# Performance work log

Hardware: AMD Instinct MI355X
Metric: run time of the kernel (lower is better)

Reference implementation:

```python
import jax, jax.numpy as jnp
import numpy as np
from jax import lax

DWT_SCALE = 0.5
IDWT_SCALE = 1.0
PAD = 2  # (kernel_size-1)//2 for k=5


def haar_dwt(x, s):
    """x: [B,C,H,W] -> (ll, lh, hl, hh) each [B,C,H/2,W/2]. 2x2 Haar, scale s."""
    a = x[..., 0::2, 0::2]
    b = x[..., 0::2, 1::2]
    c = x[..., 1::2, 0::2]
    d = x[..., 1::2, 1::2]
    ll = s * (a + b + c + d)
    lh = s * (a + b - c - d)
    hl = s * (a - b + c - d)
    hh = s * (a - b - c + d)
    return ll, lh, hl, hh


def haar_idwt(ll, lh, hl, hh, s):
    """Inverse of haar_dwt when s_dwt * s_idwt_total = 0.5. Returns [B,C,2H,2W]."""
    a = s * (ll + lh + hl + hh)
    b = s * (ll + lh - hl - hh)
    c = s * (ll - lh + hl - hh)
    d = s * (ll - lh - hl + hh)
    B, C, H2, W2 = ll.shape
    top = jnp.stack([a, b], axis=-1).reshape(B, C, H2, 2 * W2)  # even rows
    bot = jnp.stack([c, d], axis=-1).reshape(B, C, H2, 2 * W2)  # odd rows
    return jnp.stack([top, bot], axis=-2).reshape(B, C, 2 * H2, 2 * W2)


def conv2d(x, w, pad):
    return lax.conv_general_dilated(
        x, w, window_strides=(1, 1), padding=[(pad, pad), (pad, pad)],
        dimension_numbers=("NCHW", "OIHW", "NCHW"))


def setup_inputs() -> dict:
    key = jax.random.key(0)
    kx, k0, k1, k2, kb = jax.random.split(key, 5)
    C, K = 64, 5
    x = jax.random.normal(kx, (8, C, 256, 256), dtype=jnp.float32)
    # kaiming_uniform-ish small init to keep 3-level recursion numerically tame
    scale = 0.02
    w0 = jax.random.normal(k0, (4 * C, 4 * C, K, K), dtype=jnp.float32) * scale
    w1 = jax.random.normal(k1, (4 * C, 4 * C, K, K), dtype=jnp.float32) * scale
    w2 = jax.random.normal(k2, (4 * C, 4 * C, K, K), dtype=jnp.float32) * scale
    bias = jax.random.normal(kb, (C,), dtype=jnp.float32) * 0.01
    return {"x": x, "w0": w0, "w1": w1, "w2": w2, "bias": bias}


def reference(x, w0, w1, w2, bias):
    weights = [w0, w1, w2]
    idwt_s = DWT_SCALE * IDWT_SCALE  # perfect reconstruction pair
    curr = x
    ll_levels, high_levels = [], []
    for w in weights:
        ll, lh, hl, hh = haar_dwt(curr, DWT_SCALE)
        curr = ll  # pre-conv LL feeds the next level
        B, C, H2, W2 = ll.shape
        stacked = jnp.stack([ll, lh, hl, hh], axis=2).reshape(B, 4 * C, H2, W2)
        y = conv2d(stacked, w, PAD)  # [B, 4*Co, H2, W2]
        y = y.reshape(B, -1, 4, H2, W2)
        ll_levels.append(y[:, :, 0])
        high_levels.append(y[:, :, 1:])
    next_ll = jnp.zeros_like(ll_levels[-1])
    for ll_t, h_t in zip(reversed(ll_levels), reversed(high_levels)):
        ll = ll_t + next_ll
        next_ll = haar_idwt(ll, h_t[:, :, 0], h_t[:, :, 1], h_t[:, :, 2], idwt_s)
    return next_ll + bias.reshape(1, -1, 1, 1)
```

## Files before the change

### kernel.cpp

```cpp
#include <hip/hip_runtime.h>


typedef unsigned short u16;
typedef __attribute__((ext_vector_type(8))) __bf16 bf16x8;
typedef __attribute__((ext_vector_type(4))) float f32x4;

__device__ __forceinline__ u16 f2bf(float f) {
  union { float f; unsigned u; } v; v.f = f;
  unsigned r = v.u + 0x7fffu + ((v.u >> 16) & 1u);
  return (u16)(r >> 16);
}
__device__ __forceinline__ float bf2f(u16 u) {
  union { unsigned u; float f; } v; v.u = ((unsigned)u) << 16;
  return v.f;
}

typedef const unsigned int __attribute__((address_space(1)))* gas1_t;
typedef unsigned int __attribute__((address_space(3)))* gas3_t;
__device__ __forceinline__ void gload16(const void* g, void* l) {
  __builtin_amdgcn_global_load_lds((gas1_t)g, (gas3_t)l, 16, 0, 0);
}

__global__ void k_wtrans(const float* __restrict__ w, u16* __restrict__ wb) {
  int co = blockIdx.x;
  int ci = threadIdx.x;
  const float* src = w + ((long)co * 256 + ci) * 25;
  float v[25];
#pragma unroll
  for (int tp = 0; tp < 25; ++tp) v[tp] = src[tp];
#pragma unroll
  for (int tp = 0; tp < 25; ++tp)
    wb[((long)tp * 256 + co) * 256 + ci] = f2bf(v[tp]);
}

__global__ void k_border(u16* __restrict__ st, int B_, int H2, int W2) {
  int PW = W2 + 4;
  int npix = 4 * PW + 4 * H2;
  int gid = blockIdx.x * blockDim.x + threadIdx.x;
  int pid = gid >> 6, lane = gid & 63;
  if (pid >= B_ * npix) return;
  int b = pid / npix, p = pid % npix;
  int row, col;
  if (p < 2 * PW) { row = p / PW; col = p % PW; }
  else if (p < 4 * PW) { int q = p - 2 * PW; row = H2 + 2 + q / PW; col = q % PW; }
  else { int q = p - 4 * PW; row = 2 + (q >> 2); int c4 = q & 3; col = (c4 < 2) ? c4 : W2 + c4; }
  long base = (((long)b * (H2 + 4) + row) * PW + col) * 256 + lane * 4;
  *(ushort4*)(st + base) = make_ushort4(0, 0, 0, 0);
}

__global__ void k_dwt(const float* __restrict__ in, u16* __restrict__ st,
                      float* __restrict__ ll, int B_, int H2, int W2) {
  int idx = blockIdx.x * blockDim.x + threadIdx.x;
  int W2h = W2 >> 1;
  int total = B_ * 64 * H2 * W2h;
  if (idx >= total) return;
  int w2h = idx % W2h; int t2 = idx / W2h;
  int h2 = t2 % H2; t2 /= H2;
  int c = t2 % 64; int b = t2 / 64;
  int w2 = w2h * 2;
  const float* r0 = in + (((long)(b * 64 + c) * (2 * H2) + 2 * h2) * (2 * W2)) + 2 * w2;
  const float* r1 = r0 + 2 * W2;
  float4 tp = *(const float4*)r0;
  float4 bt = *(const float4*)r1;
  float ll0 = 0.5f * (tp.x + tp.y + bt.x + bt.y);
  float lh0 = 0.5f * (tp.x + tp.y - bt.x - bt.y);
  float hl0 = 0.5f * (tp.x - tp.y + bt.x - bt.y);
  float hh0 = 0.5f * (tp.x - tp.y - bt.x + bt.y);
  float ll1 = 0.5f * (tp.z + tp.w + bt.z + bt.w);
  float lh1 = 0.5f * (tp.z + tp.w - bt.z - bt.w);
  float hl1 = 0.5f * (tp.z - tp.w + bt.z - bt.w);
  float hh1 = 0.5f * (tp.z - tp.w - bt.z + bt.w);
  long sbase = (((long)b * (H2 + 4) + (h2 + 2)) * (W2 + 4) + (w2 + 2)) * 256 + 4 * c;
  *(ushort4*)(st + sbase)       = make_ushort4(f2bf(ll0), f2bf(lh0), f2bf(hl0), f2bf(hh0));
  *(ushort4*)(st + sbase + 256) = make_ushort4(f2bf(ll1), f2bf(lh1), f2bf(hl1), f2bf(hh1));
  long lbase = (((long)(b * 64 + c) * H2) + h2) * W2 + w2;
  *(float2*)(ll + lbase) = make_float2(ll0, ll1);
}

__global__ __launch_bounds__(512, 1) void k_conv8(
    const u16* __restrict__ st, const u16* __restrict__ wt, u16* __restrict__ y,
    int H2, int W2) {
  __shared__ __align__(16) char smem[131072];
  const int t = threadIdx.x;
  const int lane = t & 63;
  const int wv = t >> 6;
  const int wm = wv >> 2, wn = wv & 3;
  const int nwg = gridDim.x;
  const int bid = blockIdx.x;
  const int lb = (bid & 7) * (nwg >> 3) + (bid >> 3);
  const int m0 = lb * 256;
  const int PW = W2 + 4;

  const int trow = t >> 3;
  const int srcci = ((t & 7) ^ (trow & 7)) * 8;
  const char* baseA[4];
#pragma unroll
  for (int u = 0; u < 4; ++u) {
    int m = m0 + u * 64 + trow;
    int w = m % W2; int q = m / W2;
    int hh = q % H2; int b = q / H2;
    long sp = ((long)(b * (H2 + 4) + hh + 2) * PW + (w + 2));
    baseA[u] = (const char*)(st + sp * 256 + srcci);
  }
  const char* baseB0 = (const char*)(wt + trow * 256 + srcci);

  f32x4 acc[8][4];
#pragma unroll
  for (int i = 0; i < 8; ++i)
#pragma unroll
    for (int j = 0; j < 4; ++j) acc[i][j] = f32x4{0.f, 0.f, 0.f, 0.f};

  const int kq = (lane >> 4) * 16;
  const int sw = (lane & 7) << 4;
  const int kx0 = (kq) ^ sw;
  const int kx1 = (64 + kq) ^ sw;
  const int aBase = (wm * 128 + (lane & 15)) * 128;
  const int bBase = 32768 + (wn * 64 + (lane & 15)) * 128;

  auto stageA = [&](int kt, char* dst, int up) {
    int tap = kt >> 2, cic = kt & 3;
    int dy = tap / 5 - 2, dx = tap % 5 - 2;
    long off = ((long)(dy * PW + dx) * 256 + cic * 64) * 2;
#pragma unroll
    for (int u = up * 2; u < up * 2 + 2; ++u)
      gload16(baseA[u] + off, dst + u * 8192 + wv * 1024);
  };
  auto stageB = [&](int kt, char* dst, int up) {
    int tap = kt >> 2, cic = kt & 3;
    long off = ((long)tap * 65536 + cic * 64) * 2;
#pragma unroll
    for (int u = up * 2; u < up * 2 + 2; ++u)
      gload16(baseB0 + u * 32768 + off, dst + 32768 + u * 8192 + wv * 1024);
  };

#define QMFMA(mh, nh)                                                              \
  _Pragma("unroll") for (int i = 0; i < 4; ++i)                                    \
  _Pragma("unroll") for (int jj = 0; jj < 2; ++jj)                                 \
  _Pragma("unroll") for (int ks = 0; ks < 2; ++ks)                                 \
    acc[(mh)*4 + i][(nh)*2 + jj] = __builtin_amdgcn_mfma_f32_16x16x32_bf16(        \
        af[mh][i][ks], bfr[jj][ks], acc[(mh)*4 + i][(nh)*2 + jj], 0, 0, 0);

  stageA(0, smem, 0); stageA(0, smem, 1);
  stageB(0, smem, 0); stageB(0, smem, 1);
  stageA(1, smem + 65536, 0); stageA(1, smem + 65536, 1);
  asm volatile("s_waitcnt vmcnt(4)" ::: "memory");
  __builtin_amdgcn_s_barrier();

  for (int kt = 0; kt < 100; ++kt) {
    char* bufp = smem + (kt & 1) * 65536;
    char* altp = smem + ((kt & 1) ^ 1) * 65536;
    bf16x8 af[2][4][2], bfr[2][2];
#pragma unroll
    for (int i = 0; i < 4; ++i) {
      af[0][i][0] = *(const bf16x8*)(bufp + aBase + i * 2048 + kx0);
      af[0][i][1] = *(const bf16x8*)(bufp + aBase + i * 2048 + kx1);
    }
#pragma unroll
    for (int jj = 0; jj < 2; ++jj) {
      bfr[jj][0] = *(const bf16x8*)(bufp + bBase + jj * 2048 + kx0);
      bfr[jj][1] = *(const bf16x8*)(bufp + bBase + jj * 2048 + kx1);
    }
    if (kt + 1 < 100) stageB(kt + 1, altp, 0);
    __builtin_amdgcn_s_barrier();
    asm volatile("s_waitcnt lgkmcnt(0)" ::: "memory");
    __builtin_amdgcn_sched_barrier(0);
    __builtin_amdgcn_s_setprio(1);
    QMFMA(0, 0)
    __builtin_amdgcn_s_setprio(0);
    __builtin_amdgcn_s_barrier();
#pragma unroll
    for (int i = 0; i < 4; ++i) {
      af[1][i][0] = *(const bf16x8*)(bufp + aBase + (4 + i) * 2048 + kx0);
      af[1][i][1] = *(const bf16x8*)(bufp + aBase + (4 + i) * 2048 + kx1);
    }
    if (kt + 1 < 100) stageB(kt + 1, altp, 1);
    __builtin_amdgcn_s_barrier();
    asm volatile("s_waitcnt lgkmcnt(0)" ::: "memory");
    __builtin_amdgcn_sched_barrier(0);
    __builtin_amdgcn_s_setprio(1);
    QMFMA(1, 0)
    __builtin_amdgcn_s_setprio(0);
    __builtin_amdgcn_s_barrier();
#pragma unroll
    for (int jj = 0; jj < 2; ++jj) {
      bfr[jj][0] = *(const bf16x8*)(bufp + bBase + (2 + jj) * 2048 + kx0);
      bfr[jj][1] = *(const bf16x8*)(bufp + bBase + (2 + jj) * 2048 + kx1);
    }
    if (kt + 2 < 100) stageA(kt + 2, bufp, 0);
    __builtin_amdgcn_s_barrier();
    asm volatile("s_waitcnt lgkmcnt(0)" ::: "memory");
    __builtin_amdgcn_sched_barrier(0);
    __builtin_amdgcn_s_setprio(1);
    QMFMA(0, 1)
    __builtin_amdgcn_s_setprio(0);
    __builtin_amdgcn_s_barrier();
    if (kt + 2 < 100) stageA(kt + 2, bufp, 1);
    __builtin_amdgcn_s_barrier();
    __builtin_amdgcn_s_setprio(1);
    QMFMA(1, 1)
    __builtin_amdgcn_s_setprio(0);
    if (kt < 98) { asm volatile("s_waitcnt vmcnt(4)" ::: "memory"); }
    else if (kt == 98) { asm volatile("s_waitcnt vmcnt(0)" ::: "memory"); }
    __builtin_amdgcn_s_barrier();
  }
#undef QMFMA

#pragma unroll
  for (int i = 0; i < 8; ++i) {
    int mloc = m0 + wm * 128 + i * 16 + (lane >> 4) * 4;
#pragma unroll
    for (int j = 0; j < 4; ++j) {
      int nloc = wn * 64 + j * 16 + (lane & 15);
#pragma unroll
      for (int r = 0; r < 4; ++r)
        y[(long)(mloc + r) * 256 + nloc] = f2bf(acc[i][j][r]);
    }
  }
}

__global__ __launch_bounds__(512, 1) void k_conv_p(
    const u16* __restrict__ st, const u16* __restrict__ wt, u16* __restrict__ y,
    int H2, int W2) {
  __shared__ __align__(16) char smem[147456];
  const int t = threadIdx.x;
  const int lane = t & 63;
  const int wv = t >> 6;
  const int wm = wv >> 2;
  const int wn = wv & 3;
  const int nwg = gridDim.x;
  const int bid = blockIdx.x;
  const int lb = (bid & 7) * (nwg >> 3) + (bid >> 3);
  const int m0 = lb * 128;
  const int PW = W2 + 4;

  const int trow = t >> 3;
  const int srcci = ((t & 7) ^ (trow & 7)) * 8;
  const char* baseA[2];
  const char* baseB[4];
#pragma unroll
  for (int h = 0; h < 2; ++h) {
    int m = m0 + h * 64 + trow;
    int w = m % W2; int q = m / W2;
    int hh = q % H2; int b = q / H2;
    long sp = ((long)(b * (H2 + 4) + hh + 2) * PW + (w + 2));
    baseA[h] = (const char*)(st + sp * 256 + srcci);
  }
#pragma unroll
  for (int u = 0; u < 4; ++u) {
    int n = u * 64 + trow;
    baseB[u] = (const char*)(wt + (long)n * 256 + srcci);
  }

  f32x4 acc[4][4];
#pragma unroll
  for (int i = 0; i < 4; ++i)
#pragma unroll
    for (int j = 0; j < 4; ++j) acc[i][j] = f32x4{0.f, 0.f, 0.f, 0.f};

  const int kq = (lane >> 4) * 16;
  int aoff[2][4], boff[2][4];
#pragma unroll
  for (int ks = 0; ks < 2; ++ks)
#pragma unroll
    for (int i = 0; i < 4; ++i) {
      int ra = wm * 64 + i * 16 + (lane & 15);
      int kb = ks * 64 + kq;
      aoff[ks][i] = ra * 128 + (kb ^ ((ra & 7) << 4));
      int rb = wn * 64 + i * 16 + (lane & 15);
      boff[ks][i] = 16384 + rb * 128 + (kb ^ ((rb & 7) << 4));
    }

  auto stage_a = [&](int kt) {
    int tap = kt >> 2, cic = kt & 3;
    int dy = tap / 5 - 2, dx = tap % 5 - 2;
    long offA = ((long)(dy * PW + dx) * 256 + cic * 64) * 2;
    long offB = ((long)tap * 65536 + cic * 64) * 2;
    char* lb2 = smem + (kt % 3) * 49152 + wv * 1024;
    gload16(baseA[0] + offA, lb2);
    gload16(baseA[1] + offA, lb2 + 8192);
    gload16(baseB[0] + offB, lb2 + 16384);
  };
  auto stage_b = [&](int kt) {
    int tap = kt >> 2, cic = kt & 3;
    long offB = ((long)tap * 65536 + cic * 64) * 2;
    char* lb2 = smem + (kt % 3) * 49152 + wv * 1024;
    gload16(baseB[1] + offB, lb2 + 24576);
    gload16(baseB[2] + offB, lb2 + 32768);
    gload16(baseB[3] + offB, lb2 + 40960);
  };

  stage_a(0); stage_b(0);
  stage_a(1); stage_b(1);
  asm volatile("s_waitcnt vmcnt(6)" ::: "memory");
  __builtin_amdgcn_s_barrier();

  for (int kt = 0; kt < 100; ++kt) {
    const char* la = smem + (kt % 3) * 49152;
    const bool st2 = (kt + 2) < 100;
    bf16x8 af[4], bfr[4];
#pragma unroll
    for (int i = 0; i < 4; ++i) af[i] = *(const bf16x8*)(la + aoff[0][i]);
#pragma unroll
    for (int j = 0; j < 4; ++j) bfr[j] = *(const bf16x8*)(la + boff[0][j]);
    if (st2) stage_a(kt + 2);
    __builtin_amdgcn_s_barrier();
    asm volatile("s_waitcnt lgkmcnt(0)" ::: "memory");
    __builtin_amdgcn_sched_barrier(0);
    __builtin_amdgcn_s_setprio(1);
#pragma unroll
    for (int i = 0; i < 4; ++i)
#pragma unroll
      for (int j = 0; j < 4; ++j)
        acc[i][j] = __builtin_amdgcn_mfma_f32_16x16x32_bf16(af[i], bfr[j], acc[i][j], 0, 0, 0);
    __builtin_amdgcn_s_setprio(0);
    __builtin_amdgcn_s_barrier();
#pragma unroll
    for (int i = 0; i < 4; ++i) af[i] = *(const bf16x8*)(la + aoff[1][i]);
#pragma unroll
    for (int j = 0; j < 4; ++j) bfr[j] = *(const bf16x8*)(la + boff[1][j]);
    if (st2) stage_b(kt + 2);
    __builtin_amdgcn_s_barrier();
    asm volatile("s_waitcnt lgkmcnt(0)" ::: "memory");
    __builtin_amdgcn_sched_barrier(0);
    __builtin_amdgcn_s_setprio(1);
#pragma unroll
    for (int i = 0; i < 4; ++i)
#pragma unroll
      for (int j = 0; j < 4; ++j)
        acc[i][j] = __builtin_amdgcn_mfma_f32_16x16x32_bf16(af[i], bfr[j], acc[i][j], 0, 0, 0);
    __builtin_amdgcn_s_setprio(0);
    if (st2) {
      asm volatile("s_waitcnt vmcnt(6)" ::: "memory");
    } else if (kt + 1 < 100) {
      asm volatile("s_waitcnt vmcnt(0)" ::: "memory");
    }
    __builtin_amdgcn_s_barrier();
  }

#pragma unroll
  for (int i = 0; i < 4; ++i) {
    int mloc = m0 + wm * 64 + i * 16 + (lane >> 4) * 4;
#pragma unroll
    for (int j = 0; j < 4; ++j) {
      int nloc = wn * 64 + j * 16 + (lane & 15);
#pragma unroll
      for (int r = 0; r < 4; ++r)
        y[(long)(mloc + r) * 256 + nloc] = f2bf(acc[i][j][r]);
    }
  }
}

__global__ __launch_bounds__(256) void k_conv(
    const u16* __restrict__ st, const u16* __restrict__ wt, u16* __restrict__ y,
    int H2, int W2) {
  __shared__ __align__(16) char smem[32768];
  const int t = threadIdx.x;
  const int lane = t & 63;
  const int wv = t >> 6;
  const int wm = wv >> 1, wn = wv & 1;
  const int m0 = blockIdx.x * 128;
  const int n0 = blockIdx.y * 128;
  const int PW = W2 + 4;
  const int lsub = lane & 7;
  const int lrow8 = lane >> 3;
  const int srcci = (lsub ^ lrow8) * 8;

  const char* baseA[4];
  const char* baseB[4];
#pragma unroll
  for (int l = 0; l < 4; ++l) {
    int ml = (wv * 4 + l) * 8 + lrow8;
    int m = m0 + ml;
    int w = m % W2;
    int q = m / W2;
    int h = q % H2;
    int b = q / H2;
    long sp = ((long)(b * (H2 + 4) + h + 2) * PW + (w + 2));
    baseA[l] = (const char*)(st + sp * 256 + srcci);
    int nl = n0 + (wv * 4 + l) * 8 + lrow8;
    baseB[l] = (const char*)(wt + (long)nl * 256 + srcci);
  }

  f32x4 acc[4][4];
#pragma unroll
  for (int i = 0; i < 4; ++i)
#pragma unroll
    for (int j = 0; j < 4; ++j) acc[i][j] = f32x4{0.f, 0.f, 0.f, 0.f};

  const int arow = wm * 64 + (lane & 15);
  const int brow = wn * 64 + (lane & 15);
  const int kq = (lane >> 4) * 16;
  int aoff[2][4], boff[2][4];
#pragma unroll
  for (int ks = 0; ks < 2; ++ks)
#pragma unroll
    for (int i = 0; i < 4; ++i) {
      int ra = arow + i * 16;
      int kb = ks * 64 + kq;
      aoff[ks][i] = ra * 128 + (kb ^ ((ra & 7) << 4));
      int rb = brow + i * 16;
      boff[ks][i] = 16384 + rb * 128 + (kb ^ ((rb & 7) << 4));
    }

  for (int kk = 0; kk < 100; ++kk) {
    const int tap = kk >> 2, cic = kk & 3;
    const int dy = tap / 5 - 2, dx = tap % 5 - 2;
    const int offA = ((dy * PW + dx) * 256 + cic * 64) * 2;
    const int offB = (tap * 65536 + cic * 64) * 2;
#pragma unroll
    for (int l = 0; l < 4; ++l) {
      gload16(baseA[l] + offA, smem + (wv * 4 + l) * 1024);
      gload16(baseB[l] + offB, smem + 16384 + (wv * 4 + l) * 1024);
    }
    __syncthreads();
#pragma unroll
    for (int ks = 0; ks < 2; ++ks) {
      bf16x8 af[4], bfr[4];
#pragma unroll
      for (int i = 0; i < 4; ++i) af[i] = *(const bf16x8*)(smem + aoff[ks][i]);
#pragma unroll
      for (int j = 0; j < 4; ++j) bfr[j] = *(const bf16x8*)(smem + boff[ks][j]);
#pragma unroll
      for (int i = 0; i < 4; ++i)
#pragma unroll
        for (int j = 0; j < 4; ++j)
          acc[i][j] = __builtin_amdgcn_mfma_f32_16x16x32_bf16(af[i], bfr[j], acc[i][j], 0, 0, 0);
    }
    __syncthreads();
  }

  const long ybase = (long)m0 * 256 + n0;
#pragma unroll
  for (int i = 0; i < 4; ++i) {
    int mloc = wm * 64 + i * 16 + (lane >> 4) * 4;
#pragma unroll
    for (int j = 0; j < 4; ++j) {
      int nloc = wn * 64 + j * 16 + (lane & 15);
#pragma unroll
      for (int r = 0; r < 4; ++r)
        y[ybase + (long)(mloc + r) * 256 + nloc] = f2bf(acc[i][j][r]);
    }
  }
}

__global__ void k_idwt(const u16* __restrict__ y, const float* __restrict__ nll,
                       float* __restrict__ out, const float* __restrict__ bias,
                       int B_, int H2, int W2) {
  int idx = blockIdx.x * blockDim.x + threadIdx.x;
  int W2h = W2 >> 1;
  int total = B_ * 64 * H2 * W2h;
  if (idx >= total) return;
  int w2h = idx % W2h; int t2 = idx / W2h;
  int h2 = t2 % H2; t2 /= H2;
  int c = t2 % 64; int b = t2 / 64;
  int w2 = w2h * 2;
  long ybase = (((long)b * H2 + h2) * W2 + w2) * 256 + 4 * c;
  ushort4 q0 = *(const ushort4*)(y + ybase);
  ushort4 q1 = *(const ushort4*)(y + ybase + 256);
  float llv0 = bf2f(q0.x), lh0 = bf2f(q0.y), hl0 = bf2f(q0.z), hh0 = bf2f(q0.w);
  float llv1 = bf2f(q1.x), lh1 = bf2f(q1.y), hl1 = bf2f(q1.z), hh1 = bf2f(q1.w);
  if (nll) {
    float2 nv = *(const float2*)(nll + (((long)(b * 64 + c) * H2 + h2) * W2 + w2));
    llv0 += nv.x; llv1 += nv.y;
  }
  float bv = bias ? bias[c] : 0.f;
  float a0 = 0.5f * (llv0 + lh0 + hl0 + hh0) + bv;
  float b0 = 0.5f * (llv0 + lh0 - hl0 - hh0) + bv;
  float c0 = 0.5f * (llv0 - lh0 + hl0 - hh0) + bv;
  float d0 = 0.5f * (llv0 - lh0 - hl0 + hh0) + bv;
  float a1 = 0.5f * (llv1 + lh1 + hl1 + hh1) + bv;
  float b1 = 0.5f * (llv1 + lh1 - hl1 - hh1) + bv;
  float c1 = 0.5f * (llv1 - lh1 + hl1 - hh1) + bv;
  float d1 = 0.5f * (llv1 - lh1 - hl1 + hh1) + bv;
  long obase = (((long)(b * 64 + c) * (2 * H2) + 2 * h2) * (2 * W2)) + 2 * w2;
  *(float4*)(out + obase)          = make_float4(a0, b0, a1, b1);
  *(float4*)(out + obase + 2 * W2) = make_float4(c0, d0, c1, d1);
}

constexpr size_t WBF_SZ1 = 25ull * 256 * 256 * 2;
constexpr size_t OFF_WBF = 0;
constexpr size_t OFF_S0  = 3 * WBF_SZ1;
constexpr size_t S0_SZ   = 8ull * 132 * 132 * 256 * 2;
constexpr size_t REL_S1 = 0;
constexpr size_t S1_SZ  = 8ull * 68 * 68 * 256 * 2;
constexpr size_t REL_L1 = REL_S1 + S1_SZ;
constexpr size_t L1_SZ  = 8ull * 64 * 64 * 64 * 4;
constexpr size_t REL_S2 = REL_L1 + L1_SZ;
constexpr size_t S2_SZ  = 8ull * 36 * 36 * 256 * 2;
constexpr size_t REL_Y1 = REL_S2 + S2_SZ;
constexpr size_t Y1_SZ  = 8ull * 64 * 64 * 256 * 2;
constexpr size_t REL_Y2 = REL_Y1 + Y1_SZ;
constexpr size_t Y2_SZ  = 8ull * 32 * 32 * 256 * 2;
constexpr size_t REL_N2 = REL_Y2 + Y2_SZ;
constexpr size_t N2_SZ  = 8ull * 64 * 64 * 64 * 4;
constexpr size_t REL_L2 = REL_N2 + N2_SZ;
constexpr size_t OFF_L0 = OFF_S0 + S0_SZ;
constexpr size_t L0_SZ  = 8ull * 64 * 128 * 128 * 4;
constexpr size_t OFF_Y0 = OFF_L0 + L0_SZ;
constexpr size_t Y0_SZ  = 8ull * 128 * 128 * 256 * 2;

extern "C" void kernel_launch(void* const* d_in, const int* in_sizes, int n_in,
                              void* d_out, int out_size, void* d_ws, size_t ws_size,
                              hipStream_t stream) {
  const float* x    = (const float*)d_in[0];
  const float* w0   = (const float*)d_in[1];
  const float* w1   = (const float*)d_in[2];
  const float* w2   = (const float*)d_in[3];
  const float* bias = (const float*)d_in[4];
  float* out = (float*)d_out;
  char* ws = (char*)d_ws;

  u16* wbf0 = (u16*)(ws + OFF_WBF);
  u16* wbf1 = (u16*)(ws + OFF_WBF + WBF_SZ1);
  u16* wbf2 = (u16*)(ws + OFF_WBF + 2 * WBF_SZ1);
  u16* s0 = (u16*)(ws + OFF_S0);
  u16* s1 = (u16*)(ws + OFF_S0 + REL_S1);
  float* l1 = (float*)(ws + OFF_S0 + REL_L1);
  u16* s2 = (u16*)(ws + OFF_S0 + REL_S2);
  u16* y1 = (u16*)(ws + OFF_S0 + REL_Y1);
  u16* y2 = (u16*)(ws + OFF_S0 + REL_Y2);
  float* n2 = (float*)(ws + OFF_S0 + REL_N2);
  float* l2 = (float*)(ws + OFF_S0 + REL_L2);
  float* l0 = (float*)(ws + OFF_L0);
  float* n1 = (float*)(ws + OFF_L0);
  u16* y0 = (u16*)(ws + OFF_Y0);

  k_wtrans<<<256, 256, 0, stream>>>(w0, wbf0);
  k_wtrans<<<256, 256, 0, stream>>>(w1, wbf1);
  k_wtrans<<<256, 256, 0, stream>>>(w2, wbf2);

  k_border<<<2080, 256, 0, stream>>>(s0, 8, 128, 128);
  k_dwt<<<16384, 256, 0, stream>>>(x, s0, l0, 8, 128, 128);
  k_conv8<<<512, 512, 0, stream>>>(s0, wbf0, y0, 128, 128);

  k_border<<<1056, 256, 0, stream>>>(s1, 8, 64, 64);
  k_border<<<544, 256, 0, stream>>>(s2, 8, 32, 32);

  k_dwt<<<4096, 256, 0, stream>>>(l0, s1, l1, 8, 64, 64);
  k_conv_p<<<256, 512, 0, stream>>>(s1, wbf1, y1, 64, 64);

  k_dwt<<<1024, 256, 0, stream>>>(l1, s2, l2, 8, 32, 32);
  k_conv<<<dim3(64, 2), 256, 0, stream>>>(s2, wbf2, y2, 32, 32);

  k_idwt<<<1024, 256, 0, stream>>>(y2, nullptr, n2, nullptr, 8, 32, 32);
  k_idwt<<<4096, 256, 0, stream>>>(y1, n2, n1, nullptr, 8, 64, 64);
  k_idwt<<<16384, 256, 0, stream>>>(y0, n1, out, bias, 8, 128, 128);
}
```

Baseline: 741.6 us.

## Prefetch next k-tile fragments into registers and reorder MFMA quadrants to cut barriers

Restructures the conv GEMM main loop. LDS fragments for the next k-tile are loaded at the end of the current tile, and the quadrant order is changed so A and B fragments are reused across adjacent MFMA groups. Some barriers and full lgkmcnt waits are removed or relaxed, and per-iteration tap/div math becomes incremental offset updates. The last two iterations are peeled to drop the bounds checks. This costs more live registers and adds risk around the LDS reuse ordering.

```diff
diff --git a/kernel.cpp b/kernel.cpp
--- a/kernel.cpp
+++ b/kernel.cpp
@@ -112,98 +112,112 @@
 
   const int kq = (lane >> 4) * 16;
   const int sw = (lane & 7) << 4;
-  const int kx0 = (kq) ^ sw;
+  const int kx0 = kq ^ sw;
   const int kx1 = (64 + kq) ^ sw;
   const int aBase = (wm * 128 + (lane & 15)) * 128;
   const int bBase = 32768 + (wn * 64 + (lane & 15)) * 128;
 
-  auto stageA = [&](int kt, char* dst, int up) {
-    int tap = kt >> 2, cic = kt & 3;
-    int dy = tap / 5 - 2, dx = tap % 5 - 2;
-    long off = ((long)(dy * PW + dx) * 256 + cic * 64) * 2;
-#pragma unroll
-    for (int u = up * 2; u < up * 2 + 2; ++u)
-      gload16(baseA[u] + off, dst + u * 8192 + wv * 1024);
+  bf16x8 a0[4][2], a1[4][2], bb[2][2];
+
+  auto stageA = [&](long off, char* dst, int half) {
+    gload16(baseA[half] + off, dst + half * 8192 + wv * 1024);
+    gload16(baseA[2 + half] + off, dst + (2 + half) * 8192 + wv * 1024);
   };
-  auto stageB = [&](int kt, char* dst, int up) {
-    int tap = kt >> 2, cic = kt & 3;
-    long off = ((long)tap * 65536 + cic * 64) * 2;
-#pragma unroll
-    for (int u = up * 2; u < up * 2 + 2; ++u)
-      gload16(baseB0 + u * 32768 + off, dst + 32768 + u * 8192 + wv * 1024);
+  auto stageB = [&](long off, char* dst, int half) {
+    gload16(baseB0 + (2 * half) * 32768 + off, dst + 32768 + (2 * half) * 8192 + wv * 1024);
+    gload16(baseB0 + (2 * half + 1) * 32768 + off, dst + 32768 + (2 * half + 1) * 8192 + wv * 1024);
   };
 
-#define QMFMA(mh, nh)                                                              \
-  _Pragma("unroll") for (int i = 0; i < 4; ++i)                                    \
-  _Pragma("unroll") for (int jj = 0; jj < 2; ++jj)                                 \
-  _Pragma("unroll") for (int ks = 0; ks < 2; ++ks)                                 \
-    acc[(mh)*4 + i][(nh)*2 + jj] = __builtin_amdgcn_mfma_f32_16x16x32_bf16(        \
-        af[mh][i][ks], bfr[jj][ks], acc[(mh)*4 + i][(nh)*2 + jj], 0, 0, 0);
-
-  stageA(0, smem, 0); stageA(0, smem, 1);
+#define LDA0(P) { _Pragma("unroll") for (int i = 0; i < 4; ++i) { \
+    a0[i][0] = *(const bf16x8*)((P) + aBase + i * 2048 + kx0);    \
+    a0[i][1] = *(const bf16x8*)((P) + aBase + i * 2048 + kx1); } }
+#define LDA1(P) { _Pragma("unroll") for (int i = 0; i < 4; ++i) {        \
+    a1[i][0] = *(const bf16x8*)((P) + aBase + 8192 + i * 2048 + kx0);    \
+    a1[i][1] = *(const bf16x8*)((P) + aBase + 8192 + i * 2048 + kx1); } }
+#define LDB01(P) { _Pragma("unroll") for (int j = 0; j < 2; ++j) { \
+    bb[j][0] = *(const bf16x8*)((P) + bBase + j * 2048 + kx0);     \
+    bb[j][1] = *(const bf16x8*)((P) + bBase + j * 2048 + kx1); } }
+#define LDB23(P) { _Pragma("unroll") for (int j = 0; j < 2; ++j) {        \
+    bb[j][0] = *(const bf16x8*)((P) + bBase + 4096 + j * 2048 + kx0);     \
+    bb[j][1] = *(const bf16x8*)((P) + bBase + 4096 + j * 2048 + kx1); } }
+#define MM(I0, J0, A)                                                         \
+  _Pragma("unroll") for (int i = 0; i < 4; ++i)                               \
+  _Pragma("unroll") for (int j = 0; j < 2; ++j)                               \
+  _Pragma("unroll") for (int ks = 0; ks < 2; ++ks)                            \
+    acc[(I0) + i][(J0) + j] = __builtin_amdgcn_mfma_f32_16x16x32_bf16(        \
+        A[i][ks], bb[j][ks], acc[(I0) + i][(J0) + j], 0, 0, 0);
+
+#define KTILE(BUFP, ALTP, STGB, STGA, VMN, OFFB, OFFA)                        \
+  { char* bufp_ = (BUFP); char* altp_ = (ALTP);                               \
+                                                              \
+    LDA1(bufp_)                                                               \
+    if (STGB) stageB((OFFB), altp_, 0);                                       \
+    __builtin_amdgcn_s_barrier();                                             \
+    asm volatile("s_waitcnt lgkmcnt(8)" ::: "memory");                        \
+    __builtin_amdgcn_sched_barrier(0);                                        \
+    __builtin_amdgcn_s_setprio(1);                                            \
+    MM(0, 0, a0)                                                              \
+    __builtin_amdgcn_s_setprio(0);                                            \
+                                                              \
+    if (STGB) stageB((OFFB), altp_, 1);                                       \
+    __builtin_amdgcn_s_barrier();                                             \
+    asm volatile("s_waitcnt lgkmcnt(0)" ::: "memory");                        \
+    __builtin_amdgcn_sched_barrier(0);                                        \
+    __builtin_amdgcn_s_setprio(1);                                            \
+    MM(4, 0, a1)                                                              \
+    __builtin_amdgcn_s_setprio(0);                                            \
+    __builtin_amdgcn_sched_barrier(0);                                        \
+    LDB23(bufp_)                                                              \
+                                                              \
+    if (STGA) stageA((OFFA), bufp_, 0);                                       \
+    __builtin_amdgcn_s_barrier();                                             \
+    asm volatile("s_waitcnt lgkmcnt(0)" ::: "memory");                        \
+    __builtin_amdgcn_sched_barrier(0);                                        \
+    __builtin_amdgcn_s_setprio(1);                                            \
+    MM(4, 2, a1)                                                              \
+    __builtin_amdgcn_s_setprio(0);                                            \
+                                                              \
+    if (STGA) stageA((OFFA), bufp_, 1);                                       \
+    if ((VMN) == 4) { asm volatile("s_waitcnt vmcnt(4)" ::: "memory"); }      \
+    else if ((VMN) == 0) { asm volatile("s_waitcnt vmcnt(0)" ::: "memory"); } \
+    __builtin_amdgcn_s_barrier();                                             \
+    asm volatile("s_waitcnt lgkmcnt(0)" ::: "memory");                        \
+    __builtin_amdgcn_sched_barrier(0);                                        \
+    __builtin_amdgcn_s_setprio(1);                                            \
+    MM(0, 2, a0)                                                              \
+    __builtin_amdgcn_s_setprio(0);                                            \
+    __builtin_amdgcn_sched_barrier(0);                                        \
+    if ((VMN) >= 0) { LDA0(altp_) LDB01(altp_) }                              \
+  }
+
+  const long offA00 = ((long)(-2 * PW - 2)) * 512;
+  stageA(offA00, smem, 0); stageA(offA00, smem, 1);
   stageB(0, smem, 0); stageB(0, smem, 1);
-  stageA(1, smem + 65536, 0); stageA(1, smem + 65536, 1);
+  stageA(offA00 + 128, smem + 65536, 0); stageA(offA00 + 128, smem + 65536, 1);
   asm volatile("s_waitcnt vmcnt(4)" ::: "memory");
   __builtin_amdgcn_s_barrier();
-
-  for (int kt = 0; kt < 100; ++kt) {
+  LDA0(smem) LDB01(smem)
+
+  long offB = 128; int cB = 1;
+  long offA = offA00 + 256; int cA = 2;
+  const long aWrap = (long)PW * 512 - 2560;
+
+  for (int kt = 0; kt < 98; ++kt) {
     char* bufp = smem + (kt & 1) * 65536;
     char* altp = smem + ((kt & 1) ^ 1) * 65536;
-    bf16x8 af[2][4][2], bfr[2][2];
-#pragma unroll
-    for (int i = 0; i < 4; ++i) {
-      af[0][i][0] = *(const bf16x8*)(bufp + aBase + i * 2048 + kx0);
-      af[0][i][1] = *(const bf16x8*)(bufp + aBase + i * 2048 + kx1);
-    }
-#pragma unroll
-    for (int jj = 0; jj < 2; ++jj) {
-      bfr[jj][0] = *(const bf16x8*)(bufp + bBase + jj * 2048 + kx0);
-      bfr[jj][1] = *(const bf16x8*)(bufp + bBase + jj * 2048 + kx1);
-    }
-    if (kt + 1 < 100) stageB(kt + 1, altp, 0);
-    __builtin_amdgcn_s_barrier();
-    asm volatile("s_waitcnt lgkmcnt(0)" ::: "memory");
-    __builtin_amdgcn_sched_barrier(0);
-    __builtin_amdgcn_s_setprio(1);
-    QMFMA(0, 0)
-    __builtin_amdgcn_s_setprio(0);
-    __builtin_amdgcn_s_barrier();
-#pragma unroll
-    for (int i = 0; i < 4; ++i) {
-      af[1][i][0] = *(const bf16x8*)(bufp + aBase + (4 + i) * 2048 + kx0);
-      af[1][i][1] = *(const bf16x8*)(bufp + aBase + (4 + i) * 2048 + kx1);
-    }
-    if (kt + 1 < 100) stageB(kt + 1, altp, 1);
-    __builtin_amdgcn_s_barrier();
-    asm volatile("s_waitcnt lgkmcnt(0)" ::: "memory");
-    __builtin_amdgcn_sched_barrier(0);
-    __builtin_amdgcn_s_setprio(1);
-    QMFMA(1, 0)
-    __builtin_amdgcn_s_setprio(0);
-    __builtin_amdgcn_s_barrier();
-#pragma unroll
-    for (int jj = 0; jj < 2; ++jj) {
-      bfr[jj][0] = *(const bf16x8*)(bufp + bBase + (2 + jj) * 2048 + kx0);
-      bfr[jj][1] = *(const bf16x8*)(bufp + bBase + (2 + jj) * 2048 + kx1);
-    }
-    if (kt + 2 < 100) stageA(kt + 2, bufp, 0);
-    __builtin_amdgcn_s_barrier();
-    asm volatile("s_waitcnt lgkmcnt(0)" ::: "memory");
-    __builtin_amdgcn_sched_barrier(0);
-    __builtin_amdgcn_s_setprio(1);
-    QMFMA(0, 1)
-    __builtin_amdgcn_s_setprio(0);
-    __builtin_amdgcn_s_barrier();
-    if (kt + 2 < 100) stageA(kt + 2, bufp, 1);
-    __builtin_amdgcn_s_barrier();
-    __builtin_amdgcn_s_setprio(1);
-    QMFMA(1, 1)
-    __builtin_amdgcn_s_setprio(0);
-    if (kt < 98) { asm volatile("s_waitcnt vmcnt(4)" ::: "memory"); }
-    else if (kt == 98) { asm volatile("s_waitcnt vmcnt(0)" ::: "memory"); }
-    __builtin_amdgcn_s_barrier();
-  }
-#undef QMFMA
+    KTILE(bufp, altp, 1, 1, 4, offB, offA)
+    offB += 128; if (++cB == 4) { cB = 0; offB += 130560; }
+    offA += 128; if (++cA == 20) { cA = 0; offA += aWrap; }
+  }
+  KTILE(smem, smem + 65536, 1, 0, 0, offB, offA)
+  KTILE(smem + 65536, smem, 0, 0, -1, offB, offA)
+
+#undef KTILE
+#undef MM
+#undef LDA0
+#undef LDA1
+#undef LDB01
+#undef LDB23
 
 #pragma unroll
   for (int i = 0; i < 8; ++i) {
```

Result: faster. 715.3 us (-3.5%).
